# Kernel tuning notes

Hardware: AMD Instinct MI355X
Metric: run time of the kernel (lower is better)

Reference implementation:

```python
import jax, jax.numpy as jnp
import numpy as np

N = 50000       # nodes
E = 800000      # edges (before self-loops)
NFEAT = 256
NHID = 16       # per-head hidden dim
HEADS = 8
NCLASS = 16
NEG_SLOPE = 0.2  # PyG GATConv default leaky-relu slope


def setup_inputs() -> dict:
    key = jax.random.key(0)
    ks = jax.random.split(key, 10)
    s = 0.05  # weight scale for numerical sanity
    return {
        "x": jax.random.normal(ks[0], (N, NFEAT), jnp.float32),
        "edge_index": jax.random.randint(ks[1], (2, E), 0, N, dtype=jnp.int32),
        "W1": jax.random.normal(ks[2], (NFEAT, HEADS * NHID), jnp.float32) * s,
        "att_src1": jax.random.normal(ks[3], (HEADS, NHID), jnp.float32) * s,
        "att_dst1": jax.random.normal(ks[4], (HEADS, NHID), jnp.float32) * s,
        "b1": jnp.zeros((HEADS * NHID,), jnp.float32),
        "W2": jax.random.normal(ks[5], (HEADS * NHID, NCLASS), jnp.float32) * s,
        "att_src2": jax.random.normal(ks[6], (1, NCLASS), jnp.float32) * s,
        "att_dst2": jax.random.normal(ks[7], (1, NCLASS), jnp.float32) * s,
        "b2": jnp.zeros((NCLASS,), jnp.float32),
    }


def gat_conv(x, edge_index, W, a_src, a_dst, b, heads, out_c, concat):
    """Faithful PyG GATConv (eval mode: dropout off, add_self_loops=True)."""
    n = x.shape[0]
    loop = jnp.arange(n, dtype=edge_index.dtype)
    src = jnp.concatenate([edge_index[0], loop])  # [E+N]
    dst = jnp.concatenate([edge_index[1], loop])  # [E+N]
    h = (x @ W).reshape(n, heads, out_c)          # [N, H, C]
    # per-node attention logits
    alpha_src = jnp.einsum('nhc,hc->nh', h, a_src)  # [N, H]
    alpha_dst = jnp.einsum('nhc,hc->nh', h, a_dst)  # [N, H]
    e = jax.nn.leaky_relu(alpha_src[src] + alpha_dst[dst], NEG_SLOPE)  # [E+N, H]
    # segment softmax over incoming edges of each dst node (self-loop guarantees nonempty)
    m = jax.lax.stop_gradient(jax.ops.segment_max(e, dst, num_segments=n))
    p = jnp.exp(e - m[dst])
    denom = jax.ops.segment_sum(p, dst, num_segments=n)
    a = p / denom[dst]                              # [E+N, H]
    out = jax.ops.segment_sum(a[:, :, None] * h[src], dst, num_segments=n)  # [N, H, C]
    out = out.reshape(n, heads * out_c) if concat else out.mean(axis=1)
    return out + b


def reference(x, edge_index, W1, att_src1, att_dst1, b1, W2, att_src2, att_dst2, b2):
    h1 = jax.nn.elu(gat_conv(x, edge_index, W1, att_src1, att_dst1, b1, HEADS, NHID, True))
    return gat_conv(h1, edge_index, W2, att_src2, att_dst2, b2, 1, NCLASS, False)
```

## Files before the change

### kernel.cpp

```cpp
#include <hip/hip_runtime.h>
#include <hip/hip_bf16.h>

#define NNODES 50000
#define NEDGES 800000
#define NFEATS 256
#define NHID 16
#define HEADS 8
#define NCLS 16
#define NEG_SLOPE 0.2f
#define TOTE (NEDGES + NNODES)
#define RSTRIDE 64
#define NBUCK 196
#define NPB 256
#define BCAP 4864
#define S1_EPT 16
#define BIN_BLOCKS ((TOTE + 4095) / 4096)
#define GSTRIDE 16
#define GEMM1_BLOCKS ((NNODES + 127) / 128)

typedef __attribute__((ext_vector_type(8))) short short8;
typedef __attribute__((ext_vector_type(4))) float floatx4;

static __device__ __forceinline__ short f2bf(float f) {
    __hip_bfloat16 b = __float2bfloat16(f);
    return *reinterpret_cast<short*>(&b);
}

#define AS1 __attribute__((address_space(1)))
#define AS3 __attribute__((address_space(3)))

static __device__ __forceinline__ void ld_lds16(const void* g, void* l) {
#if __has_builtin(__builtin_amdgcn_global_load_lds)
    __builtin_amdgcn_global_load_lds((const AS1 void*)g, (AS3 void*)l, 16, 0, 0);
#endif
}


__global__ __launch_bounds__(256) void k_bin(const int* __restrict__ ei,
                                             int* __restrict__ gcnt, int* __restrict__ barr,
                                             const float* __restrict__ W,
                                             const float* __restrict__ a_s,
                                             const float* __restrict__ a_d,
                                             short* __restrict__ Wsw) {
    int tid = threadIdx.x;
    if (blockIdx.x >= BIN_BLOCKS) {
        int t = (blockIdx.x - BIN_BLOCKS) * 256 + tid;
        if (t >= 4608) return;
        short8 b;
        if (t < 4096) {
            int kc = t >> 9, nt = (t >> 6) & 7, lane = t & 63;
            int quad = lane >> 4, lo = lane & 15;
#pragma unroll
            for (int j = 0; j < 8; j++)
                b[j] = f2bf(W[(size_t)(kc * 32 + quad * 8 + j) * 128 + nt * 16 + lo]);
        } else {
            int t2 = t - 4096;
            int kc = t2 >> 6, lane = t2 & 63;
            int quad = lane >> 4, lo = lane & 15;
            int h = lo & 7;
            const float* av = (lo < 8) ? (a_s + h * 16) : (a_d + h * 16);
#pragma unroll
            for (int j = 0; j < 8; j++) {
                int k = kc * 32 + quad * 8 + j;
                float acc = 0.f;
#pragma unroll
                for (int c = 0; c < 16; c++) acc += W[(size_t)k * 128 + h * 16 + c] * av[c];
                b[j] = f2bf(acc);
            }
        }
        *(short8*)(Wsw + (size_t)t * 8) = b;
        return;
    }

    __shared__ int lcnt[NBUCK], lbase[NBUCK];
    if (tid < NBUCK) lcnt[tid] = 0;
    __syncthreads();
    int e0 = blockIdx.x * (256 * S1_EPT) + tid;
    int s[S1_EPT], d[S1_EPT], rk[S1_EPT];
#pragma unroll
    for (int k = 0; k < S1_EPT; k++) {
        int e = e0 + k * 256;
        bool v = e < TOTE;
        int ss = 0, dd = 0;
        if (v) {
            if (e < NEDGES) { ss = ei[e]; dd = ei[NEDGES + e]; }
            else            { ss = e - NEDGES; dd = ss; }
        }
        s[k] = ss; d[k] = dd;
        rk[k] = v ? atomicAdd(&lcnt[dd >> 8], 1) : -1;
    }
    __syncthreads();
    if (tid < NBUCK) lbase[tid] = lcnt[tid] ? atomicAdd(&gcnt[tid * GSTRIDE], lcnt[tid]) : 0;
    __syncthreads();
#pragma unroll
    for (int k = 0; k < S1_EPT; k++) {
        if (rk[k] >= 0) {
            int b = d[k] >> 8;
            int pos = lbase[b] + rk[k];
            if (pos < BCAP)
                barr[(size_t)b * BCAP + pos] = ((d[k] & 255) << 16) | s[k];
        }
    }
}


__global__ __launch_bounds__(256, 2) void k_mid(const int* __restrict__ gcnt,
                                             const int* __restrict__ barr,
                                             int* __restrict__ cnt, unsigned short* __restrict__ csr,
                                             const float* __restrict__ x,
                                             const short* __restrict__ Wsw,
                                             __hip_bfloat16* __restrict__ h1,
                                             float* __restrict__ as1, float* __restrict__ ad1) {
    __shared__ short smem[32768];
    int tid = threadIdx.x;

    if (blockIdx.x < NBUCK) {
        int* lcnt = (int*)smem;
        unsigned short* lcsr = (unsigned short*)smem + 512;
        int b = blockIdx.x;
        lcnt[tid] = 0;
        __syncthreads();
        int n = min(gcnt[b * GSTRIDE], BCAP);
        int nodeBase = b << 8;
        for (int i = tid; i < n; i += 256) {
            int e = barr[(size_t)b * BCAP + i];
            int ln = e >> 16;
            int r = atomicAdd(&lcnt[ln], 1);
            if (r < RSTRIDE) lcsr[ln * 65 + r] = (unsigned short)(e & 0xFFFF);
        }
        __syncthreads();
        int node = nodeBase + tid;
        if (node < NNODES) cnt[node] = min(lcnt[tid], RSTRIDE);
        for (int i = tid; i < NPB * RSTRIDE; i += 256) {
            int ln = i >> 6;
            int nn = nodeBase + ln;
            if (nn < NNODES && (i & 63) < min(lcnt[ln], RSTRIDE))
                csr[(size_t)nodeBase * RSTRIDE + i] = lcsr[ln * 65 + (i & 63)];
        }
        return;
    }

    short* bsw = smem;
    int bid  = blockIdx.x - NBUCK;
    int wave = tid >> 6;
    int lane = tid & 63;
    int quad = lane >> 4;
    int lo   = lane & 15;

    int rowBase = bid * 128 + wave * 32;
    const float* xa[2];
#pragma unroll
    for (int mt = 0; mt < 2; mt++) {
        int row = rowBase + mt * 16 + lo;
        row = (row < NNODES) ? row : (NNODES - 1);
        xa[mt] = x + (size_t)row * 256 + quad * 8;
    }

    float4 xf0[8], xf1[8], xf2[8], xf3[8];
#pragma unroll
    for (int kc = 0; kc < 8; kc++) {
        xf0[kc] = *(const float4*)(xa[0] + kc * 32);
        xf1[kc] = *(const float4*)(xa[0] + kc * 32 + 4);
        xf2[kc] = *(const float4*)(xa[1] + kc * 32);
        xf3[kc] = *(const float4*)(xa[1] + kc * 32 + 4);
    }

#if __has_builtin(__builtin_amdgcn_global_load_lds)
    {
        const char* gsrc = (const char*)Wsw + (size_t)wave * 1024 + (size_t)lane * 16;
        char* ldst = (char*)bsw + wave * 1024;
#pragma unroll
        for (int it = 0; it < 16; it++)
            ld_lds16(gsrc + it * 4096, ldst + it * 4096);
    }
#else
    {
        const uint4* g4 = (const uint4*)Wsw;
        uint4* l4 = (uint4*)bsw;
#pragma unroll
        for (int it = 0; it < 16; it++) l4[it * 256 + tid] = g4[it * 256 + tid];
    }
#endif

    short8 afr[2][8];
#pragma unroll
    for (int kc = 0; kc < 8; kc++) {
        union { short8 s; __hip_bfloat162 h[4]; } u;
        u.h[0] = __float22bfloat162_rn(make_float2(xf0[kc].x, xf0[kc].y));
        u.h[1] = __float22bfloat162_rn(make_float2(xf0[kc].z, xf0[kc].w));
        u.h[2] = __float22bfloat162_rn(make_float2(xf1[kc].x, xf1[kc].y));
        u.h[3] = __float22bfloat162_rn(make_float2(xf1[kc].z, xf1[kc].w));
        afr[0][kc] = u.s;
        u.h[0] = __float22bfloat162_rn(make_float2(xf2[kc].x, xf2[kc].y));
        u.h[1] = __float22bfloat162_rn(make_float2(xf2[kc].z, xf2[kc].w));
        u.h[2] = __float22bfloat162_rn(make_float2(xf3[kc].x, xf3[kc].y));
        u.h[3] = __float22bfloat162_rn(make_float2(xf3[kc].z, xf3[kc].w));
        afr[1][kc] = u.s;
    }

    short8 wafr[8];
#pragma unroll
    for (int kc = 0; kc < 8; kc++)
        wafr[kc] = *(const short8*)(Wsw + (size_t)(4096 + kc * 64 + lane) * 8);
    __syncthreads();

    floatx4 acc[2][8], accA[2];
#pragma unroll
    for (int mt = 0; mt < 2; mt++) {
        accA[mt] = (floatx4){0.f, 0.f, 0.f, 0.f};
#pragma unroll
        for (int nt = 0; nt < 8; nt++) acc[mt][nt] = (floatx4){0.f, 0.f, 0.f, 0.f};
    }

#pragma unroll
    for (int kc = 0; kc < 8; kc++) {
#pragma unroll
        for (int nt = 0; nt < 8; nt++) {
            short8 bfr = *(const short8*)&bsw[((kc * 8 + nt) * 64 + lane) * 8];
            acc[0][nt] = __builtin_amdgcn_mfma_f32_16x16x32_bf16(afr[0][kc], bfr, acc[0][nt], 0, 0, 0);
            acc[1][nt] = __builtin_amdgcn_mfma_f32_16x16x32_bf16(afr[1][kc], bfr, acc[1][nt], 0, 0, 0);
        }
        accA[0] = __builtin_amdgcn_mfma_f32_16x16x32_bf16(afr[0][kc], wafr[kc], accA[0], 0, 0, 0);
        accA[1] = __builtin_amdgcn_mfma_f32_16x16x32_bf16(afr[1][kc], wafr[kc], accA[1], 0, 0, 0);
    }

#pragma unroll
    for (int mt = 0; mt < 2; mt++)
#pragma unroll
        for (int nt = 0; nt < 8; nt++)
#pragma unroll
            for (int reg = 0; reg < 4; reg++) {
                int row = rowBase + mt * 16 + quad * 4 + reg;
                int col = nt * 16 + lo;
                if (row < NNODES)
                    h1[(size_t)row * 128 + col] = __float2bfloat16(acc[mt][nt][reg]);
            }
#pragma unroll
    for (int mt = 0; mt < 2; mt++)
#pragma unroll
        for (int reg = 0; reg < 4; reg++) {
            int row = rowBase + mt * 16 + quad * 4 + reg;
            if (row < NNODES) {
                float v = accA[mt][reg];
                if (lo < 8) as1[(size_t)row * 8 + lo] = v;
                else        ad1[(size_t)row * 8 + (lo - 8)] = v;
            }
        }
}


__global__ __launch_bounds__(256) void k_aggA(const int* __restrict__ cnt,
                                              const unsigned short* __restrict__ csr,
                                              const __hip_bfloat16* __restrict__ h1,
                                              const float* __restrict__ as1, const float* __restrict__ ad1,
                                              const float* __restrict__ b1,
                                              const float* __restrict__ W2,
                                              const float* __restrict__ a_s2,
                                              const float* __restrict__ a_d2,
                                              float* __restrict__ h2,
                                              float* __restrict__ as2, float* __restrict__ ad2) {
    __shared__ float w2t[16 * 132];
    __shared__ float vbuf[4 * 4 * 132];
    int tid = threadIdx.x;
#pragma unroll
    for (int i = 0; i < 8; i++) {
        int e = i * 256 + tid;
        w2t[(e & 15) * 132 + (e >> 4)] = W2[e];
    }
    __syncthreads();

    int wavid = tid >> 6;
    int lane  = tid & 63;
    int cl    = lane & 15;
    int nd    = lane >> 4;
    int node  = (blockIdx.x * 4 + wavid) * 4 + nd;
    int head  = cl >> 1;
    int deg   = min(cnt[node], RSTRIDE);
    float adst = ad1[node * 8 + head];
    int rs = node * RSTRIDE;
    int rowv[4];
#pragma unroll
    for (int r = 0; r < 4; r++) rowv[r] = csr[rs + cl + 16 * r];
    int md = deg;
    md = max(md, __shfl_xor(md, 16));
    md = max(md, __shfl_xor(md, 32));

    float acc[8] = {0.f, 0.f, 0.f, 0.f, 0.f, 0.f, 0.f, 0.f};
    float s = 0.f;
#pragma unroll
    for (int r = 0; r < 4; r++) {
        int rbase = r << 4;
        if (rbase >= md) break;
        int lim = min(16, md - rbase);
        for (int i2 = 0; i2 < lim; i2 += 4) {
            float p[4];
            union { short8 v; __hip_bfloat162 h[4]; } u[4];
#pragma unroll
            for (int t = 0; t < 4; t++) {
                int idx = rbase + i2 + t;
                int src = __shfl(rowv[r], (lane & 48) | ((i2 + t) & 15));
                p[t] = 0.f;
                u[t].v = (short8){0, 0, 0, 0, 0, 0, 0, 0};
                if (idx < deg) {
                    u[t].v = *(const short8*)(h1 + (size_t)src * 128 + cl * 8);
                    float e = as1[src * 8 + head] + adst;
                    e = (e > 0.f) ? e : NEG_SLOPE * e;
                    p[t] = __expf(e);
                }
            }
            s += (p[0] + p[1]) + (p[2] + p[3]);
#pragma unroll
            for (int t = 0; t < 4; t++)
#pragma unroll
                for (int q = 0; q < 4; q++) {
                    float2 f = __bfloat1622float2(u[t].h[q]);
                    acc[q * 2]     = fmaf(p[t], f.x, acc[q * 2]);
                    acc[q * 2 + 1] = fmaf(p[t], f.y, acc[q * 2 + 1]);
                }
        }
    }
    float is = 1.f / s;
    float v[8];
#pragma unroll
    for (int q = 0; q < 8; q++) {
        float t = acc[q] * is + b1[cl * 8 + q];
        v[q] = (t > 0.f) ? t : (__expf(t) - 1.f);
    }
    float* vb = &vbuf[(wavid * 4 + nd) * 132 + cl * 8];
    *(float4*)vb       = make_float4(v[0], v[1], v[2], v[3]);
    *(float4*)(vb + 4) = make_float4(v[4], v[5], v[6], v[7]);

    const float* vrow = &vbuf[(wavid * 4 + nd) * 132];
    const float* wrow = &w2t[cl * 132];
    float outp = 0.f;
#pragma unroll
    for (int j = 0; j < 128; j += 4) {
        float4 vv = *(const float4*)(vrow + j);
        float4 ww = *(const float4*)(wrow + j);
        outp = fmaf(vv.x, ww.x, outp);
        outp = fmaf(vv.y, ww.y, outp);
        outp = fmaf(vv.z, ww.z, outp);
        outp = fmaf(vv.w, ww.w, outp);
    }
    h2[(size_t)node * 16 + cl] = outp;

    float sv = outp * a_s2[cl];
    float dv = outp * a_d2[cl];
#pragma unroll
    for (int o = 1; o <= 8; o <<= 1) {
        sv += __shfl_xor(sv, o);
        dv += __shfl_xor(dv, o);
    }
    if (cl == 0) { as2[node] = sv; ad2[node] = dv; }
}


__global__ __launch_bounds__(256) void k_agg2(const int* __restrict__ cnt,
                                              const unsigned short* __restrict__ csr,
                                              const float* __restrict__ h2, const float* __restrict__ as2,
                                              const float* __restrict__ ad2, const float* __restrict__ b2,
                                              float* __restrict__ out) {
    int tid   = threadIdx.x;
    int wavid = tid >> 6;
    int lane  = tid & 63;
    int nd    = lane >> 4;
    int sub   = lane & 15;
    int slot  = sub >> 2;
    int c4    = sub & 3;
    int node  = (blockIdx.x * 4 + wavid) * 4 + nd;
    int deg   = min(cnt[node], RSTRIDE);
    float adst = ad2[node];
    int rs = node * RSTRIDE;
    int rowv[4];
#pragma unroll
    for (int r = 0; r < 4; r++) rowv[r] = csr[rs + sub + 16 * r];
    int md = deg;
    md = max(md, __shfl_xor(md, 16));
    md = max(md, __shfl_xor(md, 32));

    float4 acc = make_float4(0.f, 0.f, 0.f, 0.f);
    float s = 0.f;
#pragma unroll
    for (int r = 0; r < 4; r++) {
        int rbase = r << 4;
        if (rbase >= md) break;
        int lim = min(16, md - rbase);
        for (int i2 = 0; i2 < lim; i2 += 8) {
            int ia = rbase + i2 + slot;
            int ib = ia + 4;
            int sa = __shfl(rowv[r], (lane & 48) | (i2 + slot));
            int sb = __shfl(rowv[r], (lane & 48) | (i2 + 4 + slot));
            float p0 = 0.f, p1 = 0.f;
            float4 r0 = make_float4(0.f, 0.f, 0.f, 0.f);
            float4 r1 = make_float4(0.f, 0.f, 0.f, 0.f);
            if (ia < deg) {
                r0 = *(const float4*)(h2 + (size_t)sa * 16 + c4 * 4);
                float e = as2[sa] + adst;
                e = (e > 0.f) ? e : NEG_SLOPE * e;
                p0 = __expf(e);
            }
            if (ib < deg) {
                r1 = *(const float4*)(h2 + (size_t)sb * 16 + c4 * 4);
                float e = as2[sb] + adst;
                e = (e > 0.f) ? e : NEG_SLOPE * e;
                p1 = __expf(e);
            }
            s += p0 + p1;
            acc.x = fmaf(p0, r0.x, fmaf(p1, r1.x, acc.x));
            acc.y = fmaf(p0, r0.y, fmaf(p1, r1.y, acc.y));
            acc.z = fmaf(p0, r0.z, fmaf(p1, r1.z, acc.z));
            acc.w = fmaf(p0, r0.w, fmaf(p1, r1.w, acc.w));
        }
    }
#pragma unroll
    for (int o = 4; o <= 8; o <<= 1) {
        acc.x += __shfl_xor(acc.x, o);
        acc.y += __shfl_xor(acc.y, o);
        acc.z += __shfl_xor(acc.z, o);
        acc.w += __shfl_xor(acc.w, o);
        s += __shfl_xor(s, o);
    }
    if (slot == 0) {
        float is = 1.f / s;
        float4 o4;
        o4.x = acc.x * is + b2[c4 * 4 + 0];
        o4.y = acc.y * is + b2[c4 * 4 + 1];
        o4.z = acc.z * is + b2[c4 * 4 + 2];
        o4.w = acc.w * is + b2[c4 * 4 + 3];
        *(float4*)(out + (size_t)node * 16 + c4 * 4) = o4;
    }
}


extern "C" void kernel_launch(void* const* d_in, const int* in_sizes, int n_in,
                              void* d_out, int out_size, void* d_ws, size_t ws_size,
                              hipStream_t stream) {
    const float* x    = (const float*)d_in[0];
    const int*   ei   = (const int*)d_in[1];
    const float* W1   = (const float*)d_in[2];
    const float* a_s1 = (const float*)d_in[3];
    const float* a_d1 = (const float*)d_in[4];
    const float* b1   = (const float*)d_in[5];
    const float* W2   = (const float*)d_in[6];
    const float* a_s2 = (const float*)d_in[7];
    const float* a_d2 = (const float*)d_in[8];
    const float* b2   = (const float*)d_in[9];
    float* out = (float*)d_out;

    char* p = (char*)d_ws;
    auto alloc = [&](size_t bytes) -> char* {
        char* q = p;
        p += (bytes + 255) & ~(size_t)255;
        return q;
    };
    int*  gcnt = (int*)alloc((size_t)NBUCK * GSTRIDE * 4);
    int*  barr = (int*)alloc((size_t)NBUCK * BCAP * 4);
    int*  cnt  = (int*)alloc((size_t)NNODES * 4);
    unsigned short* csr = (unsigned short*)alloc((size_t)NNODES * RSTRIDE * 2);
    short* Wsw = (short*)alloc((size_t)36864 * 2);
    __hip_bfloat16* h1 = (__hip_bfloat16*)alloc((size_t)NNODES * 128 * 2);
    float* as1 = (float*)alloc((size_t)NNODES * 8 * 4);
    float* ad1 = (float*)alloc((size_t)NNODES * 8 * 4);
    float* h2  = (float*)alloc((size_t)NNODES * 16 * 4);
    float* as2 = (float*)barr;
    float* ad2 = (float*)barr + NNODES;

    hipMemsetAsync(gcnt, 0, (size_t)NBUCK * GSTRIDE * 4, stream);
    hipLaunchKernelGGL(k_bin,  dim3(BIN_BLOCKS + 18), dim3(256), 0, stream,
                       ei, gcnt, barr, W1, a_s1, a_d1, Wsw);
    hipLaunchKernelGGL(k_mid,  dim3(NBUCK + GEMM1_BLOCKS), dim3(256), 0, stream,
                       gcnt, barr, cnt, csr, x, Wsw, h1, as1, ad1);
    hipLaunchKernelGGL(k_aggA, dim3(NNODES / 16), dim3(256), 0, stream,
                       cnt, csr, h1, as1, ad1, b1, W2, a_s2, a_d2, h2, as2, ad2);
    hipLaunchKernelGGL(k_agg2, dim3(NNODES / 16), dim3(256), 0, stream, cnt, csr, h2, as2, ad2, b2, out);
}
```

Measured before the change: 185.0 us.

## Run edge binning alongside GEMM1 and compute swizzled weights per block

Merges the edge-binning kernel with the first-layer GEMM into a single launch, so binning blocks and GEMM blocks run concurrently. The CSR build moves into its own kernel that runs afterward. The pre-swizzled bf16 weight buffer is removed. Each GEMM block now converts W1 and computes the attention-projected weights itself, straight from fp32 global memory. This takes the GEMM off the binning dependency, but every GEMM block repeats the weight conversion and W·a dot products.

```diff
diff --git a/kernel.cpp b/kernel.cpp
--- a/kernel.cpp
+++ b/kernel.cpp
@@ -26,122 +26,54 @@
     return *reinterpret_cast<short*>(&b);
 }
 
-#define AS1 __attribute__((address_space(1)))
-#define AS3 __attribute__((address_space(3)))
-
-static __device__ __forceinline__ void ld_lds16(const void* g, void* l) {
-#if __has_builtin(__builtin_amdgcn_global_load_lds)
-    __builtin_amdgcn_global_load_lds((const AS1 void*)g, (AS3 void*)l, 16, 0, 0);
-#endif
-}
-
-
-__global__ __launch_bounds__(256) void k_bin(const int* __restrict__ ei,
-                                             int* __restrict__ gcnt, int* __restrict__ barr,
-                                             const float* __restrict__ W,
-                                             const float* __restrict__ a_s,
-                                             const float* __restrict__ a_d,
-                                             short* __restrict__ Wsw) {
-    int tid = threadIdx.x;
-    if (blockIdx.x >= BIN_BLOCKS) {
-        int t = (blockIdx.x - BIN_BLOCKS) * 256 + tid;
-        if (t >= 4608) return;
-        short8 b;
-        if (t < 4096) {
-            int kc = t >> 9, nt = (t >> 6) & 7, lane = t & 63;
-            int quad = lane >> 4, lo = lane & 15;
-#pragma unroll
-            for (int j = 0; j < 8; j++)
-                b[j] = f2bf(W[(size_t)(kc * 32 + quad * 8 + j) * 128 + nt * 16 + lo]);
-        } else {
-            int t2 = t - 4096;
-            int kc = t2 >> 6, lane = t2 & 63;
-            int quad = lane >> 4, lo = lane & 15;
-            int h = lo & 7;
-            const float* av = (lo < 8) ? (a_s + h * 16) : (a_d + h * 16);
-#pragma unroll
-            for (int j = 0; j < 8; j++) {
-                int k = kc * 32 + quad * 8 + j;
-                float acc = 0.f;
-#pragma unroll
-                for (int c = 0; c < 16; c++) acc += W[(size_t)k * 128 + h * 16 + c] * av[c];
-                b[j] = f2bf(acc);
-            }
-        }
-        *(short8*)(Wsw + (size_t)t * 8) = b;
-        return;
-    }
-
-    __shared__ int lcnt[NBUCK], lbase[NBUCK];
-    if (tid < NBUCK) lcnt[tid] = 0;
-    __syncthreads();
-    int e0 = blockIdx.x * (256 * S1_EPT) + tid;
-    int s[S1_EPT], d[S1_EPT], rk[S1_EPT];
-#pragma unroll
-    for (int k = 0; k < S1_EPT; k++) {
-        int e = e0 + k * 256;
-        bool v = e < TOTE;
-        int ss = 0, dd = 0;
-        if (v) {
-            if (e < NEDGES) { ss = ei[e]; dd = ei[NEDGES + e]; }
-            else            { ss = e - NEDGES; dd = ss; }
-        }
-        s[k] = ss; d[k] = dd;
-        rk[k] = v ? atomicAdd(&lcnt[dd >> 8], 1) : -1;
-    }
-    __syncthreads();
-    if (tid < NBUCK) lbase[tid] = lcnt[tid] ? atomicAdd(&gcnt[tid * GSTRIDE], lcnt[tid]) : 0;
-    __syncthreads();
-#pragma unroll
-    for (int k = 0; k < S1_EPT; k++) {
-        if (rk[k] >= 0) {
-            int b = d[k] >> 8;
-            int pos = lbase[b] + rk[k];
-            if (pos < BCAP)
-                barr[(size_t)b * BCAP + pos] = ((d[k] & 255) << 16) | s[k];
-        }
-    }
-}
-
-
-__global__ __launch_bounds__(256, 2) void k_mid(const int* __restrict__ gcnt,
-                                             const int* __restrict__ barr,
-                                             int* __restrict__ cnt, unsigned short* __restrict__ csr,
-                                             const float* __restrict__ x,
-                                             const short* __restrict__ Wsw,
-                                             __hip_bfloat16* __restrict__ h1,
-                                             float* __restrict__ as1, float* __restrict__ ad1) {
+
+__global__ __launch_bounds__(256, 2) void k_bg(const int* __restrict__ ei,
+                                               int* __restrict__ gcnt, int* __restrict__ barr,
+                                               const float* __restrict__ W,
+                                               const float* __restrict__ a_s,
+                                               const float* __restrict__ a_d,
+                                               const float* __restrict__ x,
+                                               __hip_bfloat16* __restrict__ h1,
+                                               float* __restrict__ as1, float* __restrict__ ad1) {
     __shared__ short smem[32768];
     int tid = threadIdx.x;
 
-    if (blockIdx.x < NBUCK) {
-        int* lcnt = (int*)smem;
-        unsigned short* lcsr = (unsigned short*)smem + 512;
-        int b = blockIdx.x;
-        lcnt[tid] = 0;
+    if (blockIdx.x < BIN_BLOCKS) {
+        int* lcnt  = (int*)smem;
+        int* lbase = lcnt + NBUCK;
+        if (tid < NBUCK) lcnt[tid] = 0;
         __syncthreads();
-        int n = min(gcnt[b * GSTRIDE], BCAP);
-        int nodeBase = b << 8;
-        for (int i = tid; i < n; i += 256) {
-            int e = barr[(size_t)b * BCAP + i];
-            int ln = e >> 16;
-            int r = atomicAdd(&lcnt[ln], 1);
-            if (r < RSTRIDE) lcsr[ln * 65 + r] = (unsigned short)(e & 0xFFFF);
+        int e0 = blockIdx.x * (256 * S1_EPT) + tid;
+        int s[S1_EPT], d[S1_EPT], rk[S1_EPT];
+#pragma unroll
+        for (int k = 0; k < S1_EPT; k++) {
+            int e = e0 + k * 256;
+            bool v = e < TOTE;
+            int ss = 0, dd = 0;
+            if (v) {
+                if (e < NEDGES) { ss = ei[e]; dd = ei[NEDGES + e]; }
+                else            { ss = e - NEDGES; dd = ss; }
+            }
+            s[k] = ss; d[k] = dd;
+            rk[k] = v ? atomicAdd(&lcnt[dd >> 8], 1) : -1;
         }
         __syncthreads();
-        int node = nodeBase + tid;
-        if (node < NNODES) cnt[node] = min(lcnt[tid], RSTRIDE);
-        for (int i = tid; i < NPB * RSTRIDE; i += 256) {
-            int ln = i >> 6;
-            int nn = nodeBase + ln;
-            if (nn < NNODES && (i & 63) < min(lcnt[ln], RSTRIDE))
-                csr[(size_t)nodeBase * RSTRIDE + i] = lcsr[ln * 65 + (i & 63)];
+        if (tid < NBUCK) lbase[tid] = lcnt[tid] ? atomicAdd(&gcnt[tid * GSTRIDE], lcnt[tid]) : 0;
+        __syncthreads();
+#pragma unroll
+        for (int k = 0; k < S1_EPT; k++) {
+            if (rk[k] >= 0) {
+                int b = d[k] >> 8;
+                int pos = lbase[b] + rk[k];
+                if (pos < BCAP)
+                    barr[(size_t)b * BCAP + pos] = ((d[k] & 255) << 16) | s[k];
+            }
         }
         return;
     }
 
     short* bsw = smem;
-    int bid  = blockIdx.x - NBUCK;
+    int bid  = blockIdx.x - BIN_BLOCKS;
     int wave = tid >> 6;
     int lane = tid & 63;
     int quad = lane >> 4;
@@ -165,22 +97,43 @@
         xf3[kc] = *(const float4*)(xa[1] + kc * 32 + 4);
     }
 
-#if __has_builtin(__builtin_amdgcn_global_load_lds)
+#pragma unroll
+    for (int it = 0; it < 16; it++) {
+        int e = it * 256 + tid;
+        int kc_e = e >> 9, nt_e = (e >> 6) & 7, ln_e = e & 63;
+        int q_e = ln_e >> 4, lo_e = ln_e & 15;
+        short8 b;
+#pragma unroll
+        for (int j = 0; j < 8; j++)
+            b[j] = f2bf(W[(size_t)(kc_e * 32 + q_e * 8 + j) * 128 + nt_e * 16 + lo_e]);
+        *(short8*)(bsw + (size_t)e * 8) = b;
+    }
+
+    short8 wafr[8];
     {
-        const char* gsrc = (const char*)Wsw + (size_t)wave * 1024 + (size_t)lane * 16;
-        char* ldst = (char*)bsw + wave * 1024;
-#pragma unroll
-        for (int it = 0; it < 16; it++)
-            ld_lds16(gsrc + it * 4096, ldst + it * 4096);
-    }
-#else
-    {
-        const uint4* g4 = (const uint4*)Wsw;
-        uint4* l4 = (uint4*)bsw;
-#pragma unroll
-        for (int it = 0; it < 16; it++) l4[it * 256 + tid] = g4[it * 256 + tid];
-    }
-#endif
+        int h = lo & 7;
+        const float* av = (lo < 8) ? (a_s + h * 16) : (a_d + h * 16);
+        float4 av0 = *(const float4*)(av);
+        float4 av1 = *(const float4*)(av + 4);
+        float4 av2 = *(const float4*)(av + 8);
+        float4 av3 = *(const float4*)(av + 12);
+#pragma unroll
+        for (int kc = 0; kc < 8; kc++) {
+            short8 b;
+#pragma unroll
+            for (int j = 0; j < 8; j++) {
+                int k = kc * 32 + quad * 8 + j;
+                const float4* wr = (const float4*)(W + (size_t)k * 128 + h * 16);
+                float4 w0 = wr[0], w1 = wr[1], w2 = wr[2], w3 = wr[3];
+                float acc = w0.x * av0.x + w0.y * av0.y + w0.z * av0.z + w0.w * av0.w
+                          + w1.x * av1.x + w1.y * av1.y + w1.z * av1.z + w1.w * av1.w
+                          + w2.x * av2.x + w2.y * av2.y + w2.z * av2.z + w2.w * av2.w
+                          + w3.x * av3.x + w3.y * av3.y + w3.z * av3.z + w3.w * av3.w;
+                b[j] = f2bf(acc);
+            }
+            wafr[kc] = b;
+        }
+    }
 
     short8 afr[2][8];
 #pragma unroll
@@ -197,11 +150,6 @@
         u.h[3] = __float22bfloat162_rn(make_float2(xf3[kc].z, xf3[kc].w));
         afr[1][kc] = u.s;
     }
-
-    short8 wafr[8];
-#pragma unroll
-    for (int kc = 0; kc < 8; kc++)
-        wafr[kc] = *(const short8*)(Wsw + (size_t)(4096 + kc * 64 + lane) * 8);
     __syncthreads();
 
     floatx4 acc[2][8], accA[2];
@@ -246,6 +194,34 @@
                 else        ad1[(size_t)row * 8 + (lo - 8)] = v;
             }
         }
+}
+
+
+__global__ __launch_bounds__(256) void k_csr(const int* __restrict__ gcnt,
+                                             const int* __restrict__ barr,
+                                             int* __restrict__ cnt, unsigned short* __restrict__ csr) {
+    __shared__ int lcnt[NPB];
+    __shared__ unsigned short lcsr[NPB * 65];
+    int b = blockIdx.x, tid = threadIdx.x;
+    lcnt[tid] = 0;
+    __syncthreads();
+    int n = min(gcnt[b * GSTRIDE], BCAP);
+    int nodeBase = b << 8;
+    for (int i = tid; i < n; i += 256) {
+        int e = barr[(size_t)b * BCAP + i];
+        int ln = e >> 16;
+        int r = atomicAdd(&lcnt[ln], 1);
+        if (r < RSTRIDE) lcsr[ln * 65 + r] = (unsigned short)(e & 0xFFFF);
+    }
+    __syncthreads();
+    int node = nodeBase + tid;
+    if (node < NNODES) cnt[node] = min(lcnt[tid], RSTRIDE);
+    for (int i = tid; i < NPB * RSTRIDE; i += 256) {
+        int ln = i >> 6;
+        int nn = nodeBase + ln;
+        if (nn < NNODES && (i & 63) < min(lcnt[ln], RSTRIDE))
+            csr[(size_t)nodeBase * RSTRIDE + i] = lcsr[ln * 65 + (i & 63)];
+    }
 }
 
 
@@ -457,7 +433,6 @@
     int*  barr = (int*)alloc((size_t)NBUCK * BCAP * 4);
     int*  cnt  = (int*)alloc((size_t)NNODES * 4);
     unsigned short* csr = (unsigned short*)alloc((size_t)NNODES * RSTRIDE * 2);
-    short* Wsw = (short*)alloc((size_t)36864 * 2);
     __hip_bfloat16* h1 = (__hip_bfloat16*)alloc((size_t)NNODES * 128 * 2);
     float* as1 = (float*)alloc((size_t)NNODES * 8 * 4);
     float* ad1 = (float*)alloc((size_t)NNODES * 8 * 4);
@@ -466,10 +441,9 @@
     float* ad2 = (float*)barr + NNODES;
 
     hipMemsetAsync(gcnt, 0, (size_t)NBUCK * GSTRIDE * 4, stream);
-    hipLaunchKernelGGL(k_bin,  dim3(BIN_BLOCKS + 18), dim3(256), 0, stream,
-                       ei, gcnt, barr, W1, a_s1, a_d1, Wsw);
-    hipLaunchKernelGGL(k_mid,  dim3(NBUCK + GEMM1_BLOCKS), dim3(256), 0, stream,
-                       gcnt, barr, cnt, csr, x, Wsw, h1, as1, ad1);
+    hipLaunchKernelGGL(k_bg,   dim3(BIN_BLOCKS + GEMM1_BLOCKS), dim3(256), 0, stream,
+                       ei, gcnt, barr, W1, a_s1, a_d1, x, h1, as1, ad1);
+    hipLaunchKernelGGL(k_csr,  dim3(NBUCK), dim3(256), 0, stream, gcnt, barr, cnt, csr);
     hipLaunchKernelGGL(k_aggA, dim3(NNODES / 16), dim3(256), 0, stream,
                        cnt, csr, h1, as1, ad1, b1, W2, a_s2, a_d2, h2, as2, ad2);
     hipLaunchKernelGGL(k_agg2, dim3(NNODES / 16), dim3(256), 0, stream, cnt, csr, h2, as2, ad2, b2, out);
```

Result: slower. 215.1 us (+16.3%).
